# Optimization experiments

Hardware: AMD Instinct MI355X
Metric: run time of the kernel (lower is better)

The kernel has to match this reference:

```python
import jax, jax.numpy as jnp
from jax import lax
import numpy as np

B, S, D, H, A = 128, 512, 256, 256, 64


def setup_inputs() -> dict:
    key = jax.random.key(0)
    ks = jax.random.split(key, 20)
    inp = {"x": jax.random.normal(ks[0], (B, S, D), jnp.float32)}
    names = ["Wih_f0", "Whh_f0", "bih_f0", "bhh_f0",
             "Wih_f1", "Whh_f1", "bih_f1", "bhh_f1",
             "Wih_b0", "Whh_b0", "bih_b0", "bhh_b0",
             "Wih_b1", "Whh_b1", "bih_b1", "bhh_b1"]
    shapes = {"Wih_f0": (4 * H, D), "Wih_b0": (4 * H, D),
              "Wih_f1": (4 * H, H), "Wih_b1": (4 * H, H)}
    for i, n in enumerate(names):
        if n.startswith("W"):
            shp = shapes.get(n, (4 * H, H))
        else:
            shp = (4 * H,)
        inp[n] = jax.random.normal(ks[i + 1], shp, jnp.float32) * 0.1
    inp["Wa1"] = jax.random.normal(ks[17], (A, 2 * H), jnp.float32) * 0.1
    inp["Wa2"] = jax.random.normal(ks[18], (1, A), jnp.float32) * 0.1
    return inp


def lstm_layer(xs, Wih, Whh, bih, bhh):
    # xs: [B, S, in] -> hidden states [B, S, H], h0=c0=0 (matches torch LSTMCell gate order i,f,g,o)
    b = xs.shape[0]
    h0 = jnp.zeros((b, Whh.shape[1]), xs.dtype)

    def step(carry, x_t):
        h, c = carry
        g = x_t @ Wih.T + bih + h @ Whh.T + bhh  # [B, 4H]
        i, f, gg, o = jnp.split(g, 4, axis=-1)
        c = jax.nn.sigmoid(f) * c + jax.nn.sigmoid(i) * jnp.tanh(gg)
        h = jax.nn.sigmoid(o) * jnp.tanh(c)
        return (h, c), h

    _, hs = lax.scan(step, (h0, h0), jnp.swapaxes(xs, 0, 1))  # [S, B, H]
    return jnp.swapaxes(hs, 0, 1)


def reference(x, Wih_f0, Whh_f0, bih_f0, bhh_f0, Wih_f1, Whh_f1, bih_f1, bhh_f1,
              Wih_b0, Whh_b0, bih_b0, bhh_b0, Wih_b1, Whh_b1, bih_b1, bhh_b1,
              Wa1, Wa2):
    # layer 0
    f = lstm_layer(x, Wih_f0, Whh_f0, bih_f0, bhh_f0)
    b = lstm_layer(x[:, ::-1], Wih_b0, Whh_b0, bih_b0, bhh_b0)[:, ::-1]
    # layer 1 (fwd stack consumes fwd states, bwd stack consumes bwd states, as in source)
    f = lstm_layer(f, Wih_f1, Whh_f1, bih_f1, bhh_f1)
    b = lstm_layer(b[:, ::-1], Wih_b1, Whh_b1, bih_b1, bhh_b1)[:, ::-1]
    out = jnp.concatenate([f, b], axis=2)  # [B, S, 2H]
    # self-attention pooling: softmax_s(Wa2 tanh(Wa1 out)) weighted sum
    scores = jnp.tanh(out @ Wa1.T) @ Wa2.T  # [B, S, 1]
    w = jax.nn.softmax(scores, axis=1)
    return jnp.sum(out * w, axis=1)  # [B, 2H]
```

## Files before the change

kernel.cpp:

```cpp
#include <hip/hip_runtime.h>
#include <stdint.h>

typedef __attribute__((ext_vector_type(8))) __bf16 bf16x8;
typedef __attribute__((ext_vector_type(4))) float  f32x4;

#define SCOPE_AGENT __HIP_MEMORY_SCOPE_AGENT
#define MFMA16(a,b,c) __builtin_amdgcn_mfma_f32_16x16x32_bf16(a,b,c,0,0,0)

__device__ __forceinline__ float sigm(float x){ return 1.0f/(1.0f + __expf(-x)); }
__device__ __forceinline__ float tanh_s(float x){
  float a = fabsf(x);
  float e = __expf(2.0f*a);
  float t = 1.0f - 2.0f/(e + 1.0f);
  return x < 0.0f ? -t : t;
}

__device__ __forceinline__ bf16x8 cvt_hi(const float4& a, const float4& b){
  bf16x8 r;
  r[0]=(__bf16)a.x; r[1]=(__bf16)a.y; r[2]=(__bf16)a.z; r[3]=(__bf16)a.w;
  r[4]=(__bf16)b.x; r[5]=(__bf16)b.y; r[6]=(__bf16)b.z; r[7]=(__bf16)b.w;
  return r;
}
__device__ __forceinline__ bf16x8 cvt_lo(const float4& a, const float4& b, bf16x8 hi){
  bf16x8 r;
  r[0]=(__bf16)(a.x-(float)hi[0]); r[1]=(__bf16)(a.y-(float)hi[1]);
  r[2]=(__bf16)(a.z-(float)hi[2]); r[3]=(__bf16)(a.w-(float)hi[3]);
  r[4]=(__bf16)(b.x-(float)hi[4]); r[5]=(__bf16)(b.y-(float)hi[5]);
  r[6]=(__bf16)(b.z-(float)hi[6]); r[7]=(__bf16)(b.w-(float)hi[7]);
  return r;
}

__global__ void fill_sentinel(float* p, int n){
  int i = blockIdx.x*blockDim.x + threadIdx.x;
  if(i < n) p[i] = 12345.0f;
}

template<bool LAYER0>
__global__ __launch_bounds__(512) void lstm_fused(
    const float*  __restrict__ xf,
    const __bf16* __restrict__ hin,
    const float* __restrict__ WihF, const float* __restrict__ WihB,
    const float* __restrict__ WhhF, const float* __restrict__ WhhB,
    const float* __restrict__ bihF, const float* __restrict__ bhhF,
    const float* __restrict__ bihB, const float* __restrict__ bhhB,
    __bf16* __restrict__ hout,
    unsigned int* __restrict__ flags)
{
  const int tid  = threadIdx.x;
  const int wave = tid>>6, lane = tid&63;
  const int bid  = blockIdx.x;
  const int dir  = bid>>5;
  const int bg   = (bid>>2)&7;
  const int q    = bid&3;

  const float* Wih = dir ? WihB : WihF;
  const float* Whh = dir ? WhhB : WhhF;
  const float* bih = dir ? bihB : bihF;
  const float* bhh = dir ? bhhB : bhhF;
  const __bf16* hinD = LAYER0 ? (const __bf16*)0 : (hin + (size_t)dir*(65536ull*256ull));
  __bf16* houtD = hout + (size_t)dir*(65536ull*256ull);
  unsigned int* myFlag = flags + (size_t)bid*32;

  __shared__ __attribute__((aligned(16))) __bf16 xsh[16*256];
  __shared__ __attribute__((aligned(16))) __bf16 xsl[16*256];
  __shared__ __attribute__((aligned(16))) __bf16 hs [16*256];
  __shared__ __attribute__((aligned(16))) float  gb [16*256];

  for(int i=tid;i<512;i+=512) *(uint4*)((char*)hs + i*16) = make_uint4(0,0,0,0);

  bf16x8 Bwh[2][8], Bwih[2][8], Bwil[2][8];
  float  bias[2];
#pragma unroll
  for(int j=0;j<2;++j){
    int nt = wave*2 + j;
    int gate = nt>>2, sub = nt&3;
    int col = gate*256 + q*64 + sub*16 + (lane&15);
    bias[j] = bih[col] + bhh[col];
    const float* wh = Whh + (size_t)col*256 + (lane>>4)*8;
    const float* wi = Wih + (size_t)col*256 + (lane>>4)*8;
#pragma unroll
    for(int kb=0;kb<8;++kb){
      float4 h0 = *(const float4*)(wh + kb*32);
      float4 h1 = *(const float4*)(wh + kb*32 + 4);
      Bwh[j][kb] = cvt_hi(h0, h1);
      float4 i0 = *(const float4*)(wi + kb*32);
      float4 i1 = *(const float4*)(wi + kb*32 + 4);
      bf16x8 hi = cvt_hi(i0, i1);
      Bwih[j][kb] = hi;
      Bwil[j][kb] = cvt_lo(i0, i1, hi);
    }
  }

  const int srow = tid>>5;
  const int sc8  = (tid&31)*8;
  const int b0r  = bg*16;
  const int urow = tid>>5;
  const int ulc  = (tid&31)*2;
  const int m    = lane&15;
  const int kq   = (lane>>4)*16;

  float c0 = 0.f, c1 = 0.f;
  __syncthreads();

  for(int t=0; t<512; ++t){
    if constexpr(LAYER0){
      int tx = dir ? (511-t) : t;
      const float* src = xf + (((size_t)(b0r+srow))*512 + tx)*256 + sc8;
      float4 xa = *(const float4*)src;
      float4 xb = *(const float4*)(src+4);
      bf16x8 hi = cvt_hi(xa, xb);
      bf16x8 lo = cvt_lo(xa, xb, hi);
      int off = srow*512 + ((sc8*2) ^ ((srow&7)<<4));
      *(bf16x8*)((char*)xsh + off) = hi;
      *(bf16x8*)((char*)xsl + off) = lo;
    } else {
      bf16x8 xv = *(const bf16x8*)(hinD + (((size_t)bg*512 + t)*16 + srow)*256 + sc8);
      *(bf16x8*)((char*)xsh + srow*512 + ((sc8*2) ^ ((srow&7)<<4))) = xv;
    }
    if(t>0 && tid<3){
      int p = tid + (tid>=q ? 1 : 0);
      unsigned int* pf = flags + (size_t)(dir*32 + bg*4 + p)*32;
      while(__hip_atomic_load(pf, __ATOMIC_ACQUIRE, SCOPE_AGENT) < (unsigned)t)
        __builtin_amdgcn_s_sleep(1);
    }
    __syncthreads();

    bf16x8 pv; int pOff = 0;
    if(t>0 && tid<384){
      int pi  = tid>>7;
      int p   = pi + (pi>=q ? 1 : 0);
      int row = (tid>>3)&15;
      int l8  = tid&7;
      int coll = p*64 + l8*8;
      pv = *(const bf16x8*)(houtD + (((size_t)bg*512 + (t-1))*16 + row)*256 + coll);
      pOff = row*512 + ((coll*2) ^ ((row&7)<<4));
    }
    f32x4 ax0 = {bias[0],bias[0],bias[0],bias[0]};
    f32x4 ax1 = {bias[1],bias[1],bias[1],bias[1]};
#pragma unroll
    for(int kb=0;kb<8;++kb){
      int off = m*512 + ((kb*64 + kq) ^ ((m&7)<<4));
      bf16x8 ah = *(const bf16x8*)((const char*)xsh + off);
      ax0 = MFMA16(ah, Bwih[0][kb], ax0);
      ax1 = MFMA16(ah, Bwih[1][kb], ax1);
      ax0 = MFMA16(ah, Bwil[0][kb], ax0);
      ax1 = MFMA16(ah, Bwil[1][kb], ax1);
      if constexpr(LAYER0){
        bf16x8 al = *(const bf16x8*)((const char*)xsl + off);
        ax0 = MFMA16(al, Bwih[0][kb], ax0);
        ax1 = MFMA16(al, Bwih[1][kb], ax1);
      }
    }
    if(t>0 && tid<384)
      *(bf16x8*)((char*)hs + pOff) = pv;
    __syncthreads();

    f32x4 ah0 = {0.f,0.f,0.f,0.f};
    f32x4 ah1 = {0.f,0.f,0.f,0.f};
#pragma unroll
    for(int kb=0;kb<8;++kb){
      int off = m*512 + ((kb*64 + kq) ^ ((m&7)<<4));
      bf16x8 hv = *(const bf16x8*)((const char*)hs + off);
      ah0 = MFMA16(hv, Bwh[0][kb], ah0);
      ah1 = MFMA16(hv, Bwh[1][kb], ah1);
    }
#pragma unroll
    for(int j=0;j<2;++j){
      int nt = wave*2 + j;
      int gate = nt>>2, sub = nt&3;
      int lc = gate*64 + sub*16 + m;
#pragma unroll
      for(int i=0;i<4;++i){
        float v = (j ? ax1[i]+ah1[i] : ax0[i]+ah0[i]);
        gb[((lane>>4)*4+i)*256 + lc] = v;
      }
    }
    __syncthreads();
    float2 ig = *(const float2*)(gb + urow*256 +   0 + ulc);
    float2 fg = *(const float2*)(gb + urow*256 +  64 + ulc);
    float2 gg = *(const float2*)(gb + urow*256 + 128 + ulc);
    float2 og = *(const float2*)(gb + urow*256 + 192 + ulc);
    c0 = sigm(fg.x)*c0 + sigm(ig.x)*tanh_s(gg.x);
    c1 = sigm(fg.y)*c1 + sigm(ig.y)*tanh_s(gg.y);
    float h0v = sigm(og.x)*tanh_s(c0);
    float h1v = sigm(og.y)*tanh_s(c1);
    union{ __bf16 b[2]; unsigned int u; } hq;
    hq.b[0] = (__bf16)h0v; hq.b[1] = (__bf16)h1v;
    int gc = q*64 + ulc;
    *(unsigned int*)((char*)hs + urow*512 + ((gc*2) ^ ((urow&7)<<4))) = hq.u;
    __hip_atomic_store((unsigned int*)(houtD + (((size_t)bg*512 + t)*16 + urow)*256 + gc),
                       hq.u, __ATOMIC_RELAXED, SCOPE_AGENT);
    __syncthreads();
    if(tid==0)
      __hip_atomic_store(myFlag, (unsigned)(t+1), __ATOMIC_RELEASE, SCOPE_AGENT);
  }
}

__global__ __launch_bounds__(512) void attn_pool(
    const __bf16* __restrict__ h1,
    const float*  __restrict__ Wa1,
    const float*  __restrict__ Wa2,
    float* __restrict__ out)
{
  __shared__ __attribute__((aligned(16))) __bf16 Ws[64*256];
  __shared__ float scoreL[512];
  __shared__ float red[16];
  const int tid = threadIdx.x, wave = tid>>6, lane = tid&63;
  const int b = blockIdx.x, bg = b>>4, rb = b&15;
  const __bf16* h1F = h1;
  const __bf16* h1B = h1 + (size_t)65536*256;

  float wa2v[4];
#pragma unroll
  for(int ni=0;ni<4;++ni) wa2v[ni] = Wa2[ni*16 + (lane&15)];

  f32x4 acc[4][4];
#pragma unroll
  for(int mi=0;mi<4;++mi)
#pragma unroll
    for(int ni=0;ni<4;++ni) acc[mi][ni] = f32x4{0.f,0.f,0.f,0.f};

  for(int it=0; it<32; ++it){
    int idx = it*512 + tid;
    int n = idx>>8, k = idx&255;
    *(__bf16*)((char*)Ws + n*512 + ((k*2) ^ ((n&7)<<4))) = (__bf16)Wa1[n*512 + k];
  }
  __syncthreads();
#pragma unroll
  for(int mi=0;mi<4;++mi){
    int tA = (wave*4+mi)*16 + (lane&15);
    const __bf16* arow = h1F + (((size_t)bg*512 + tA)*16 + rb)*256;
#pragma unroll
    for(int kb=0;kb<8;++kb){
      int kk = kb*32 + (lane>>4)*8;
      bf16x8 a = *(const bf16x8*)(arow + kk);
#pragma unroll
      for(int ni=0;ni<4;++ni){
        int n = ni*16 + (lane&15);
        bf16x8 w = *(const bf16x8*)((const char*)Ws + n*512 + ((kk*2) ^ ((n&7)<<4)));
        acc[mi][ni] = MFMA16(a, w, acc[mi][ni]);
      }
    }
  }
  __syncthreads();
  for(int it=0; it<32; ++it){
    int idx = it*512 + tid;
    int n = idx>>8, k = idx&255;
    *(__bf16*)((char*)Ws + n*512 + ((k*2) ^ ((n&7)<<4))) = (__bf16)Wa1[n*512 + 256 + k];
  }
  __syncthreads();
#pragma unroll
  for(int mi=0;mi<4;++mi){
    int tA = (wave*4+mi)*16 + (lane&15);
    const __bf16* arow = h1B + (((size_t)bg*512 + (511-tA))*16 + rb)*256;
#pragma unroll
    for(int kb=0;kb<8;++kb){
      int kk = kb*32 + (lane>>4)*8;
      bf16x8 a = *(const bf16x8*)(arow + kk);
#pragma unroll
      for(int ni=0;ni<4;++ni){
        int n = ni*16 + (lane&15);
        bf16x8 w = *(const bf16x8*)((const char*)Ws + n*512 + ((kk*2) ^ ((n&7)<<4)));
        acc[mi][ni] = MFMA16(a, w, acc[mi][ni]);
      }
    }
  }
#pragma unroll
  for(int mi=0;mi<4;++mi){
    float sp[4] = {0.f,0.f,0.f,0.f};
#pragma unroll
    for(int ni=0;ni<4;++ni)
#pragma unroll
      for(int i=0;i<4;++i) sp[i] += tanh_s(acc[mi][ni][i]) * wa2v[ni];
#pragma unroll
    for(int i=0;i<4;++i){
      float v = sp[i];
      v += __shfl_xor(v, 1, 64); v += __shfl_xor(v, 2, 64);
      v += __shfl_xor(v, 4, 64); v += __shfl_xor(v, 8, 64);
      if((lane&15) == 0) scoreL[(wave*4+mi)*16 + (lane>>4)*4 + i] = v;
    }
  }
  __syncthreads();
  float sv = scoreL[tid];
  float mx = sv;
  for(int o=32;o>=1;o>>=1) mx = fmaxf(mx, __shfl_xor(mx, o, 64));
  if(lane==0) red[wave] = mx;
  __syncthreads();
  if(tid==0){ float mm=red[0]; for(int i=1;i<8;++i) mm=fmaxf(mm,red[i]); red[8]=mm; }
  __syncthreads();
  mx = red[8];
  float e = __expf(sv - mx);
  float ss = e;
  for(int o=32;o>=1;o>>=1) ss += __shfl_xor(ss, o, 64);
  if(lane==0) red[wave] = ss;
  __syncthreads();
  if(tid==0){ float s2=0.f; for(int i=0;i<8;++i) s2+=red[i]; red[9]=s2; }
  __syncthreads();
  float wgt = e / red[9];
  scoreL[tid] = wgt;
  __syncthreads();
  const int j = tid;
  const bool bwd = (j >= 256);
  const int jj = bwd ? (j - 256) : j;
  const __bf16* hsrc = bwd ? h1B : h1F;
  float a0=0.f,a1=0.f,a2=0.f,a3=0.f;
  for(int t=0;t<512;t+=4){
#pragma unroll
    for(int u=0;u<4;++u){
      int tt = t + u;
      size_t tr = bwd ? (size_t)(511 - tt) : (size_t)tt;
      float val = (float)hsrc[(((size_t)bg*512 + tr)*16 + rb)*256 + jj];
      float wt = scoreL[tt];
      if(u==0) a0 += wt*val; else if(u==1) a1 += wt*val;
      else if(u==2) a2 += wt*val; else a3 += wt*val;
    }
  }
  out[(size_t)b*512 + j] = (a0+a1)+(a2+a3);
}

#define H_BYTES 67108864ull

extern "C" void kernel_launch(void* const* d_in, const int* in_sizes, int n_in,
                              void* d_out, int out_size, void* d_ws, size_t ws_size,
                              hipStream_t stream)
{
  (void)in_sizes; (void)n_in;
  const float* x     = (const float*)d_in[0];
  const float* WihF0 = (const float*)d_in[1];
  const float* WhhF0 = (const float*)d_in[2];
  const float* bihF0 = (const float*)d_in[3];
  const float* bhhF0 = (const float*)d_in[4];
  const float* WihF1 = (const float*)d_in[5];
  const float* WhhF1 = (const float*)d_in[6];
  const float* bihF1 = (const float*)d_in[7];
  const float* bhhF1 = (const float*)d_in[8];
  const float* WihB0 = (const float*)d_in[9];
  const float* WhhB0 = (const float*)d_in[10];
  const float* bihB0 = (const float*)d_in[11];
  const float* bhhB0 = (const float*)d_in[12];
  const float* WihB1 = (const float*)d_in[13];
  const float* WhhB1 = (const float*)d_in[14];
  const float* bihB1 = (const float*)d_in[15];
  const float* bhhB1 = (const float*)d_in[16];
  const float* Wa1   = (const float*)d_in[17];
  const float* Wa2   = (const float*)d_in[18];
  float* out = (float*)d_out;

  if(ws_size < 2*H_BYTES + 16384){
    fill_sentinel<<<(out_size+255)/256, 256, 0, stream>>>(out, out_size);
    return;
  }

  char* ws = (char*)d_ws;
  __bf16* h0 = (__bf16*)ws;
  __bf16* h1 = (__bf16*)(ws + H_BYTES);
  unsigned int* flags = (unsigned int*)(ws + 2*H_BYTES);

  hipMemsetAsync(flags, 0, 16384, stream);

  lstm_fused<true ><<<64, 512, 0, stream>>>(
      x, (const __bf16*)0,
      WihF0, WihB0, WhhF0, WhhB0, bihF0, bhhF0, bihB0, bhhB0,
      h0, flags);
  lstm_fused<false><<<64, 512, 0, stream>>>(
      (const float*)0, h0,
      WihF1, WihB1, WhhF1, WhhB1, bihF1, bhhF1, bihB1, bhhB1,
      h1, flags + 2048);
  attn_pool<<<128, 512, 0, stream>>>(h1, Wa1, Wa2, out);
}
```

Before: 3.634 ms.

## Run both LSTM layers concurrently in one kernel with per-timestep flag pipelining

Merges the layer-0 and layer-1 recurrent kernels into a single 128-block launch. Layer-1 blocks spin on the layer-0 flags for the same batch group and direction, so layer 1 advances a wavefront behind layer 0 instead of waiting for it to finish. Also prefetches the next timestep's x into registers, moves each peer-flag wait onto lane 0 of the wave that reads that peer, paired with an acquire fence, and pads the gate buffer stride to reduce LDS bank conflicts. It depends on all 128 blocks being co-resident, since spinning blocks would deadlock otherwise, and it adds cross-layer polling traffic.

New measurement: 6.019 ms. 1.66x slower.

```diff
diff --git a/kernel.cpp b/kernel.cpp
--- a/kernel.cpp
+++ b/kernel.cpp
@@ -35,36 +35,23 @@
   if(i < n) p[i] = 12345.0f;
 }
 
+#define GB_STRIDE 260
+
 template<bool LAYER0>
-__global__ __launch_bounds__(512) void lstm_fused(
+__device__ __forceinline__ void lstm_body(
     const float*  __restrict__ xf,
-    const __bf16* __restrict__ hin,
-    const float* __restrict__ WihF, const float* __restrict__ WihB,
-    const float* __restrict__ WhhF, const float* __restrict__ WhhB,
-    const float* __restrict__ bihF, const float* __restrict__ bhhF,
-    const float* __restrict__ bihB, const float* __restrict__ bhhB,
-    __bf16* __restrict__ hout,
-    unsigned int* __restrict__ flags)
+    const __bf16* __restrict__ hinD,
+    const float* __restrict__ Wih, const float* __restrict__ Whh,
+    const float* __restrict__ bih, const float* __restrict__ bhh,
+    __bf16* __restrict__ houtD,
+    unsigned int* __restrict__ lflags,
+    const unsigned int* __restrict__ gate4,
+    int dir, int bg, int q,
+    __bf16* xsh, __bf16* xsl, __bf16* hs, float* gb)
 {
   const int tid  = threadIdx.x;
   const int wave = tid>>6, lane = tid&63;
-  const int bid  = blockIdx.x;
-  const int dir  = bid>>5;
-  const int bg   = (bid>>2)&7;
-  const int q    = bid&3;
-
-  const float* Wih = dir ? WihB : WihF;
-  const float* Whh = dir ? WhhB : WhhF;
-  const float* bih = dir ? bihB : bihF;
-  const float* bhh = dir ? bhhB : bhhF;
-  const __bf16* hinD = LAYER0 ? (const __bf16*)0 : (hin + (size_t)dir*(65536ull*256ull));
-  __bf16* houtD = hout + (size_t)dir*(65536ull*256ull);
-  unsigned int* myFlag = flags + (size_t)bid*32;
-
-  __shared__ __attribute__((aligned(16))) __bf16 xsh[16*256];
-  __shared__ __attribute__((aligned(16))) __bf16 xsl[16*256];
-  __shared__ __attribute__((aligned(16))) __bf16 hs [16*256];
-  __shared__ __attribute__((aligned(16))) float  gb [16*256];
+  unsigned int* myFlag = lflags + (size_t)(dir*32 + bg*4 + q)*32;
 
   for(int i=tid;i<512;i+=512) *(uint4*)((char*)hs + i*16) = make_uint4(0,0,0,0);
 
@@ -80,9 +67,9 @@
     const float* wi = Wih + (size_t)col*256 + (lane>>4)*8;
 #pragma unroll
     for(int kb=0;kb<8;++kb){
-      float4 h0 = *(const float4*)(wh + kb*32);
-      float4 h1 = *(const float4*)(wh + kb*32 + 4);
-      Bwh[j][kb] = cvt_hi(h0, h1);
+      float4 h0v4 = *(const float4*)(wh + kb*32);
+      float4 h1v4 = *(const float4*)(wh + kb*32 + 4);
+      Bwh[j][kb] = cvt_hi(h0v4, h1v4);
       float4 i0 = *(const float4*)(wi + kb*32);
       float4 i1 = *(const float4*)(wi + kb*32 + 4);
       bf16x8 hi = cvt_hi(i0, i1);
@@ -93,48 +80,64 @@
 
   const int srow = tid>>5;
   const int sc8  = (tid&31)*8;
-  const int b0r  = bg*16;
   const int urow = tid>>5;
   const int ulc  = (tid&31)*2;
   const int m    = lane&15;
   const int kq   = (lane>>4)*16;
 
   float c0 = 0.f, c1 = 0.f;
+
+  float4 pxa = {0,0,0,0}, pxb = {0,0,0,0};
+  if constexpr(LAYER0){
+    int tx = dir ? 511 : 0;
+    const float* src = xf + (((size_t)(bg*16+srow))*512 + tx)*256 + sc8;
+    pxa = *(const float4*)src; pxb = *(const float4*)(src+4);
+  }
   __syncthreads();
 
   for(int t=0; t<512; ++t){
     if constexpr(LAYER0){
-      int tx = dir ? (511-t) : t;
-      const float* src = xf + (((size_t)(b0r+srow))*512 + tx)*256 + sc8;
-      float4 xa = *(const float4*)src;
-      float4 xb = *(const float4*)(src+4);
-      bf16x8 hi = cvt_hi(xa, xb);
-      bf16x8 lo = cvt_lo(xa, xb, hi);
+      bf16x8 hi = cvt_hi(pxa, pxb);
+      bf16x8 lo = cvt_lo(pxa, pxb, hi);
       int off = srow*512 + ((sc8*2) ^ ((srow&7)<<4));
       *(bf16x8*)((char*)xsh + off) = hi;
       *(bf16x8*)((char*)xsl + off) = lo;
     } else {
+      if(lane < 4){
+        const unsigned int* gf = gate4 + lane*32;
+        while(__hip_atomic_load(gf, __ATOMIC_RELAXED, SCOPE_AGENT) < (unsigned)(t+1))
+          __builtin_amdgcn_s_sleep(1);
+      }
+      __builtin_amdgcn_fence(__ATOMIC_ACQUIRE, "agent");
       bf16x8 xv = *(const bf16x8*)(hinD + (((size_t)bg*512 + t)*16 + srow)*256 + sc8);
       *(bf16x8*)((char*)xsh + srow*512 + ((sc8*2) ^ ((srow&7)<<4))) = xv;
     }
-    if(t>0 && tid<3){
-      int p = tid + (tid>=q ? 1 : 0);
-      unsigned int* pf = flags + (size_t)(dir*32 + bg*4 + p)*32;
-      while(__hip_atomic_load(pf, __ATOMIC_ACQUIRE, SCOPE_AGENT) < (unsigned)t)
-        __builtin_amdgcn_s_sleep(1);
-    }
     __syncthreads();
 
+    if constexpr(LAYER0){
+      int tn = (t+1 < 512) ? (t+1) : 511;
+      int tx = dir ? (511-tn) : tn;
+      const float* src = xf + (((size_t)(bg*16+srow))*512 + tx)*256 + sc8;
+      pxa = *(const float4*)src; pxb = *(const float4*)(src+4);
+    }
+
     bf16x8 pv; int pOff = 0;
-    if(t>0 && tid<384){
-      int pi  = tid>>7;
-      int p   = pi + (pi>=q ? 1 : 0);
+    if(t>0 && wave<6){
+      int pw = wave>>1;
+      int p  = pw + (pw>=q ? 1 : 0);
+      if(lane==0){
+        const unsigned int* pf = lflags + (size_t)(dir*32 + bg*4 + p)*32;
+        while(__hip_atomic_load(pf, __ATOMIC_RELAXED, SCOPE_AGENT) < (unsigned)t)
+          __builtin_amdgcn_s_sleep(1);
+      }
+      __builtin_amdgcn_fence(__ATOMIC_ACQUIRE, "agent");
       int row = (tid>>3)&15;
       int l8  = tid&7;
       int coll = p*64 + l8*8;
       pv = *(const bf16x8*)(houtD + (((size_t)bg*512 + (t-1))*16 + row)*256 + coll);
       pOff = row*512 + ((coll*2) ^ ((row&7)<<4));
     }
+
     f32x4 ax0 = {bias[0],bias[0],bias[0],bias[0]};
     f32x4 ax1 = {bias[1],bias[1],bias[1],bias[1]};
 #pragma unroll
@@ -151,7 +154,7 @@
         ax1 = MFMA16(al, Bwih[1][kb], ax1);
       }
     }
-    if(t>0 && tid<384)
+    if(t>0 && wave<6)
       *(bf16x8*)((char*)hs + pOff) = pv;
     __syncthreads();
 
@@ -172,14 +175,14 @@
 #pragma unroll
       for(int i=0;i<4;++i){
         float v = (j ? ax1[i]+ah1[i] : ax0[i]+ah0[i]);
-        gb[((lane>>4)*4+i)*256 + lc] = v;
+        gb[((lane>>4)*4+i)*GB_STRIDE + lc] = v;
       }
     }
     __syncthreads();
-    float2 ig = *(const float2*)(gb + urow*256 +   0 + ulc);
-    float2 fg = *(const float2*)(gb + urow*256 +  64 + ulc);
-    float2 gg = *(const float2*)(gb + urow*256 + 128 + ulc);
-    float2 og = *(const float2*)(gb + urow*256 + 192 + ulc);
+    float2 ig = *(const float2*)(gb + urow*GB_STRIDE +   0 + ulc);
+    float2 fg = *(const float2*)(gb + urow*GB_STRIDE +  64 + ulc);
+    float2 gg = *(const float2*)(gb + urow*GB_STRIDE + 128 + ulc);
+    float2 og = *(const float2*)(gb + urow*GB_STRIDE + 192 + ulc);
     c0 = sigm(fg.x)*c0 + sigm(ig.x)*tanh_s(gg.x);
     c1 = sigm(fg.y)*c1 + sigm(ig.y)*tanh_s(gg.y);
     float h0v = sigm(og.x)*tanh_s(c0);
@@ -193,6 +196,50 @@
     __syncthreads();
     if(tid==0)
       __hip_atomic_store(myFlag, (unsigned)(t+1), __ATOMIC_RELEASE, SCOPE_AGENT);
+  }
+}
+
+__global__ __launch_bounds__(512) void lstm_both(
+    const float* __restrict__ xf,
+    const float* __restrict__ WihF0, const float* __restrict__ WihB0,
+    const float* __restrict__ WhhF0, const float* __restrict__ WhhB0,
+    const float* __restrict__ bihF0, const float* __restrict__ bhhF0,
+    const float* __restrict__ bihB0, const float* __restrict__ bhhB0,
+    const float* __restrict__ WihF1, const float* __restrict__ WihB1,
+    const float* __restrict__ WhhF1, const float* __restrict__ WhhB1,
+    const float* __restrict__ bihF1, const float* __restrict__ bhhF1,
+    const float* __restrict__ bihB1, const float* __restrict__ bhhB1,
+    __bf16* __restrict__ h0, __bf16* __restrict__ h1,
+    unsigned int* __restrict__ flags)
+{
+  __shared__ __attribute__((aligned(16))) __bf16 xsh[16*256];
+  __shared__ __attribute__((aligned(16))) __bf16 xsl[16*256];
+  __shared__ __attribute__((aligned(16))) __bf16 hs [16*256];
+  __shared__ __attribute__((aligned(16))) float  gb [16*GB_STRIDE];
+
+  const int bid = blockIdx.x;
+  const int b6  = bid & 63;
+  const int dir = (b6>>5)&1;
+  const int bg  = (b6>>2)&7;
+  const int q   = b6&3;
+
+  if(bid < 64){
+    lstm_body<true>(
+        xf, (const __bf16*)0,
+        dir ? WihB0 : WihF0, dir ? WhhB0 : WhhF0,
+        dir ? bihB0 : bihF0, dir ? bhhB0 : bhhF0,
+        h0 + (size_t)dir*(65536ull*256ull),
+        flags, (const unsigned int*)0,
+        dir, bg, q, xsh, xsl, hs, gb);
+  } else {
+    lstm_body<false>(
+        (const float*)0, h0 + (size_t)dir*(65536ull*256ull),
+        dir ? WihB1 : WihF1, dir ? WhhB1 : WhhF1,
+        dir ? bihB1 : bihF1, dir ? bhhB1 : bhhF1,
+        h1 + (size_t)dir*(65536ull*256ull),
+        flags + 2048,
+        flags + (size_t)(dir*32 + bg*4)*32,
+        dir, bg, q, xsh, xsl, hs, gb);
   }
 }
 
@@ -358,13 +405,10 @@
 
   hipMemsetAsync(flags, 0, 16384, stream);
 
-  lstm_fused<true ><<<64, 512, 0, stream>>>(
-      x, (const __bf16*)0,
+  lstm_both<<<128, 512, 0, stream>>>(
+      x,
       WihF0, WihB0, WhhF0, WhhB0, bihF0, bhhF0, bihB0, bhhB0,
-      h0, flags);
-  lstm_fused<false><<<64, 512, 0, stream>>>(
-      (const float*)0, h0,
       WihF1, WihB1, WhhF1, WhhB1, bihF1, bhhF1, bihB1, bhhB1,
-      h1, flags + 2048);
+      h0, h1, flags);
   attn_pool<<<128, 512, 0, stream>>>(h1, Wa1, Wa2, out);
 }
```
